# Kernel tuning notes

Hardware: AMD Instinct MI355X
Metric: run time of the kernel (lower is better)

The kernel has to match this reference:

```python
import jax, jax.numpy as jnp
import numpy as np

N_EX, N_KC, D, HID, NHEADS = 10000, 500, 128, 128, 2
B, S = 256, 500
ALPHA = 0.2
NEG = -9e15


def setup_inputs() -> dict:
    key = jax.random.key(0)
    ks = jax.random.split(key, 24)
    sc = 0.1
    inp = {
        "adj_exercise_kc": jax.random.randint(ks[0], (N_EX, N_KC), 0, 2, dtype=jnp.int32),
        "kc_data": jax.random.randint(ks[1], (B, S), 0, N_KC).astype(jnp.int64),
        "exercise_data": jax.random.randint(ks[2], (B, S), 0, N_EX + 1).astype(jnp.int64),
        "exercise_respond_data": jax.random.randint(ks[3], (B, S), 0, 2 * N_EX + 1).astype(jnp.int64),
        "target": jax.random.randint(ks[4], (B * (S - 1), 1), 0, 2).astype(jnp.float32),
        # learned parameters
        "ex_embed": jax.random.normal(ks[5], (N_EX, D)) * sc,
        "kc_embed": jax.random.normal(ks[6], (N_KC, D)) * sc,
        "W1": jax.random.normal(ks[7], (NHEADS, D, D)) * sc,        # per-head shared proj
        "a_att": jax.random.normal(ks[8], (NHEADS, 2 * D, 1)) * sc,  # attention vector
        "E": jax.random.normal(ks[9], (NHEADS, D, D)) * sc,
        "rd_w": jax.random.normal(ks[10], (NHEADS, D, 2 * D)) * sc,  # reduceDim (mode 3)
        "rd_b": jnp.zeros((NHEADS, D)),
        "w_ih": jax.random.normal(ks[11], (4 * HID, 2 * D)) * sc,
        "w_hh": jax.random.normal(ks[12], (4 * HID, HID)) * sc,
        "b_ih": jnp.zeros((4 * HID,)),
        "b_hh": jnp.zeros((4 * HID,)),
        "fc1_w": jax.random.normal(ks[13], (HID, D + HID)) * sc,
        "fc1_b": jnp.zeros((HID,)),
        "fc2_w": jax.random.normal(ks[14], (1, HID)) * sc,
        "fc2_b": jnp.zeros((1,)),
    }
    return inp


def _gat_head(ex_h, kc_h, adj, W1h, ah, Eh, rdw, rdb):
    # mode == 3 GAT head. a_input @ a decomposes: e[i,j] = LReLU(exWh[i].a1 + kcWh[j].a2)
    kc_Wh = kc_h @ W1h                                   # [Nkc, D]
    ex_Wh = ex_h @ W1h                                   # [Nex, D]
    e = jax.nn.leaky_relu(ex_Wh @ ah[:D] + (kc_Wh @ ah[D:]).T, ALPHA)  # [Nex, Nkc]
    att = jax.nn.softmax(jnp.where(adj > 0, e, NEG), axis=1)
    new_kc = att @ kc_Wh                                 # [Nex, D]
    ex_Eh = ex_h @ Eh
    emb = jnp.concatenate([new_kc, new_kc * ex_Eh], axis=1) @ rdw.T + rdb
    return jax.nn.elu(emb)                               # [Nex, D]


def _lstm(x, w_ih, w_hh, b_ih, b_hh):
    # single-layer torch LSTM, gate order i,f,g,o
    b = x.shape[0]
    xg = jnp.einsum('bsi,gi->sbg', x, w_ih) + b_ih + b_hh  # [S,B,4H]

    def step(carry, xt):
        h, c = carry
        g = xt + h @ w_hh.T
        i, f, gg, o = jnp.split(g, 4, axis=-1)
        c = jax.nn.sigmoid(f) * c + jax.nn.sigmoid(i) * jnp.tanh(gg)
        h = jax.nn.sigmoid(o) * jnp.tanh(c)
        return (h, c), h

    init = (jnp.zeros((b, HID), x.dtype), jnp.zeros((b, HID), x.dtype))
    _, hs = jax.lax.scan(step, init, xg)
    return jnp.swapaxes(hs, 0, 1)                        # [B,S,H]


def _forward(adj, exercise_data, respond_data, target,
             ex_embed, kc_embed, W1, a_att, E, rd_w, rd_b,
             w_ih, w_hh, b_ih, b_hh, fc1_w, fc1_b, fc2_w, fc2_b):
    heads = jax.vmap(_gat_head, in_axes=(None, None, None, 0, 0, 0, 0, 0))(
        ex_embed, kc_embed, adj, W1, a_att, E, rd_w, rd_b)   # [NH, Nex, D]
    # torch: cat(dim=1).view(Nex, D, NH).mean(2) -> interleaved reshape of the concat
    cat = jnp.swapaxes(heads, 0, 1).reshape(N_EX, NHEADS * D)
    exercise_embedding = cat.reshape(N_EX, D, NHEADS).mean(-1)  # [Nex, D]

    emb0 = jnp.concatenate([jnp.zeros((1, D), exercise_embedding.dtype), exercise_embedding], 0)
    assess = emb0[exercise_data]                          # [B,S,D]

    zeros = jnp.zeros_like(exercise_embedding)
    resp_emb = jnp.concatenate([
        jnp.concatenate([zeros, exercise_embedding], -1),
        jnp.concatenate([exercise_embedding, zeros], -1)], 0)  # [2Nex, 2D]
    resp0 = jnp.concatenate([jnp.zeros((1, 2 * D), resp_emb.dtype), resp_emb], 0)
    lstm_input = resp0[respond_data]                      # [B,S,2D]

    learn = _lstm(lstm_input, w_ih, w_hh, b_ih, b_hh)[:, :S - 1, :]  # [B,S-1,H]
    assess = assess[:, 1:, :]                             # [B,S-1,D]

    y = jax.nn.relu(jnp.concatenate([learn, assess], -1) @ fc1_w.T + fc1_b)
    pred = (y @ fc2_w.T + fc2_b).reshape(-1)              # [B*(S-1)]
    t = target.reshape(-1)                                # all targets >= 0 => mask all-true
    # BCE with logits, mean reduction
    loss = jnp.mean(jnp.maximum(pred, 0) - pred * t + jnp.log1p(jnp.exp(-jnp.abs(pred))))
    return loss, jax.nn.sigmoid(pred), t


def reference(adj_exercise_kc, kc_data, exercise_data, exercise_respond_data, target,
              ex_embed, kc_embed, W1, a_att, E, rd_w, rd_b,
              w_ih, w_hh, b_ih, b_hh, fc1_w, fc1_b, fc2_w, fc2_b):
    del kc_data  # unused by the original forward body
    return _forward(adj_exercise_kc, exercise_data, exercise_respond_data, target,
                    ex_embed, kc_embed, W1, a_att, E, rd_w, rd_b,
                    w_ih, w_hh, b_ih, b_hh, fc1_w, fc1_b, fc2_w, fc2_b)
```

## Files before the change

kernel.cpp:

```cpp
#include <hip/hip_runtime.h>
#include <math.h>

#define N_EX 10000
#define N_KC 500
#define D 128
#define HID 128
#define BB 256
#define SS 500
#define NROWS 127744

typedef float vf4 __attribute__((ext_vector_type(4)));
typedef _Float16 hf2 __attribute__((ext_vector_type(2)));

__device__ __forceinline__ float sigm(float x) { return 1.f / (1.f + __expf(-x)); }
__device__ __forceinline__ float tanh_fast(float x) { return 1.f - 2.f / (1.f + __expf(2.f * x)); }

__device__ __forceinline__ hf2 u2h(unsigned v) { union { unsigned u; hf2 h; } x; x.u = v; return x.h; }

__device__ __forceinline__ float quad_sum(float x) {
    int a = __builtin_amdgcn_update_dpp(0, __float_as_int(x), 0xB1, 0xF, 0xF, true);
    x += __int_as_float(a);
    int b = __builtin_amdgcn_update_dpp(0, __float_as_int(x), 0x4E, 0xF, 0xF, true);
    x += __int_as_float(b);
    return x;
}

__global__ void k_precomp(const float* rd_w, const float* w_ih, const float* fc1_w,
                          const float* b_ih, const float* b_hh, const float* W1, const float* a_att,
                          const float* w_hh,
                          float* rd_wT, float* w_ihT0, float* w_ihT1,
                          float* fc1_AT, float* fc1_BT, float* v1,
                          unsigned short* wlstm16, float* projC) {
    int idx = blockIdx.x * blockDim.x + threadIdx.x;
    int stride = gridDim.x * blockDim.x;
    const int N1 = 2 * 256 * 128;
    const int N2 = 128 * 512;
    const int N3 = 128 * 512;
    const int N4 = 128 * 128;
    const int N5 = 128 * 128;
    const int N6 = 512;
    const int N7 = 256;
    const int N8 = 65536;
    int total = N1 + N2 + N3 + N4 + N5 + N6 + N7 + N8;
    for (int tt = idx; tt < total; tt += stride) {
        int u = tt;
        if (u < N1) {
            int h = u / (256 * 128); int rem = u % (256 * 128); int c = rem / 128; int dd = rem % 128;
            rd_wT[u] = rd_w[h * 128 * 256 + dd * 256 + c];
        } else if ((u -= N1) < N2) {
            int k = u / 512, g = u % 512; w_ihT0[u] = w_ih[g * 256 + k];
        } else if ((u -= N2) < N3) {
            int k = u / 512, g = u % 512; w_ihT1[u] = w_ih[g * 256 + 128 + k];
        } else if ((u -= N3) < N4) {
            int k = u / 128, j = u % 128; fc1_AT[u] = fc1_w[j * 256 + k];
        } else if ((u -= N4) < N5) {
            int k = u / 128, j = u % 128; fc1_BT[u] = fc1_w[j * 256 + 128 + k];
        } else if ((u -= N5) < N6) {
            projC[u] = b_ih[u] + b_hh[u];
        } else if ((u -= N6) < N7) {
            int h = u / 128, k = u % 128;
            const float* wr = W1 + h * 16384 + k * 128;
            const float* av = a_att + h * 256;
            float acc = 0.f;
            for (int d = 0; d < 128; ++d) acc += wr[d] * av[d];
            v1[u] = acc;
        } else {
            u -= N7;
            int x = u & 7;
            int t = (u >> 3) & 511;
            int i = u >> 12;
            int g = i >> 2, j = i & 3;
            int uu = t >> 2, q = t & 3;
            float val = w_hh[(g * 128 + uu) * 128 + q * 32 + j * 8 + x];
            ((_Float16*)wlstm16)[u] = (_Float16)val;
        }
    }
}

__global__ void k_kc(const float* kc_embed, const float* W1, const float* a_att,
                     float* kcWhT, float* s_kc) {
    int j = blockIdx.x, h = blockIdx.y, d = threadIdx.x;
    __shared__ float row[128];
    __shared__ float red[128];
    row[d] = kc_embed[j * 128 + d];
    __syncthreads();
    const float* w = W1 + h * 16384;
    float acc = 0.f;
    for (int k = 0; k < 128; ++k) acc += row[k] * w[k * 128 + d];
    kcWhT[((size_t)(h * 128 + d)) * 500 + j] = acc;
    red[d] = acc * a_att[h * 256 + 128 + d];
    __syncthreads();
    for (int s = 64; s > 0; s >>= 1) { if (d < s) red[d] += red[d + s]; __syncthreads(); }
    if (d == 0) s_kc[h * 500 + j] = red[0];
}

__global__ void k_sex(const float* ex_embed, const float* v1, float* s_ex) {
    int t = blockIdx.x * blockDim.x + threadIdx.x;
    if (t >= 2 * N_EX) return;
    int h = t / N_EX, i = t % N_EX;
    const float4* e4 = (const float4*)(ex_embed + (size_t)i * 128);
    const float4* v4 = (const float4*)(v1 + h * 128);
    float acc = 0.f;
    for (int k = 0; k < 32; ++k) {
        float4 a = e4[k], b = v4[k];
        acc += a.x * b.x + a.y * b.y + a.z * b.z + a.w * b.w;
    }
    s_ex[h * N_EX + i] = acc;
}

__global__ __launch_bounds__(256) void k_attnk(const int* adj, const float* s_ex, const float* s_kc,
                                               const float* kcWhT, float* new_kc) {
    int i0 = blockIdx.x * 8, t = threadIdx.x;
    __shared__ vf4 at4[2][1500];
    __shared__ float skc_l[2][500];
    float* at0 = (float*)at4[0];
    float* at1 = (float*)at4[1];
    for (int j = t; j < 1000; j += 256) ((float*)skc_l)[j] = s_kc[j];
    __syncthreads();
    {
        int lg = t >> 5, lane = t & 31;
        int i = i0 + lg;
        float sex0 = s_ex[i];
        float sex1 = s_ex[N_EX + i];
        const int* arow = adj + (size_t)i * 500;
        float lmax0 = -INFINITY, lmax1 = -INFINITY;
        for (int j = lane; j < 500; j += 32) {
            bool m = arow[j] > 0;
            float e0 = sex0 + skc_l[0][j];
            e0 = (e0 >= 0.f) ? e0 : 0.2f * e0;
            e0 = m ? e0 : -INFINITY;
            float e1 = sex1 + skc_l[1][j];
            e1 = (e1 >= 0.f) ? e1 : 0.2f * e1;
            e1 = m ? e1 : -INFINITY;
            at0[j * 12 + lg] = e0;
            at1[j * 12 + lg] = e1;
            lmax0 = fmaxf(lmax0, e0);
            lmax1 = fmaxf(lmax1, e1);
        }
#pragma unroll
        for (int m = 16; m > 0; m >>= 1) {
            lmax0 = fmaxf(lmax0, __shfl_xor(lmax0, m));
            lmax1 = fmaxf(lmax1, __shfl_xor(lmax1, m));
        }
        float lsum0 = 0.f, lsum1 = 0.f;
        for (int j = lane; j < 500; j += 32) {
            float w0 = __expf(at0[j * 12 + lg] - lmax0);
            float w1 = __expf(at1[j * 12 + lg] - lmax1);
            at0[j * 12 + lg] = w0;
            at1[j * 12 + lg] = w1;
            lsum0 += w0; lsum1 += w1;
        }
#pragma unroll
        for (int m = 16; m > 0; m >>= 1) {
            lsum0 += __shfl_xor(lsum0, m);
            lsum1 += __shfl_xor(lsum1, m);
        }
        float inv0 = 1.f / lsum0, inv1 = 1.f / lsum1;
        for (int j = lane; j < 500; j += 32) {
            at0[j * 12 + lg] *= inv0;
            at1[j * 12 + lg] *= inv1;
        }
    }
    __syncthreads();
    int d = t & 127, half = t >> 7;
    for (int h = 0; h < 2; ++h) {
        const float* at = (h == 0) ? at0 : at1;
        const float* kcwd = kcWhT + ((size_t)(h * 128 + d)) * 500;
        vf4 acc = {0.f, 0.f, 0.f, 0.f};
        for (int j4 = 0; j4 < 125; ++j4) {
            vf4 w = *(const vf4*)(kcwd + j4 * 4);
            vf4 a0 = *(const vf4*)(at + (j4 * 4 + 0) * 12 + half * 4);
            vf4 a1 = *(const vf4*)(at + (j4 * 4 + 1) * 12 + half * 4);
            vf4 a2 = *(const vf4*)(at + (j4 * 4 + 2) * 12 + half * 4);
            vf4 a3 = *(const vf4*)(at + (j4 * 4 + 3) * 12 + half * 4);
            acc += a0 * w.x + a1 * w.y + a2 * w.z + a3 * w.w;
        }
        new_kc[((size_t)h * N_EX + i0 + half * 4 + 0) * 128 + d] = acc.x;
        new_kc[((size_t)h * N_EX + i0 + half * 4 + 1) * 128 + d] = acc.y;
        new_kc[((size_t)h * N_EX + i0 + half * 4 + 2) * 128 + d] = acc.z;
        new_kc[((size_t)h * N_EX + i0 + half * 4 + 3) * 128 + d] = acc.w;
    }
}

__global__ __launch_bounds__(256) void k_gat2m(const float* new_kc, const float* ex_embed,
                                               const float* E, const float* rd_wT,
                                               const float* rd_b, float* emb_e) {
    int i0 = blockIdx.x * 8, t = threadIdx.x;
    int d = t & 127, half = t >> 7;
    __shared__ float exrT[128 * 8];
    __shared__ float nkT[2][128 * 8];
    __shared__ float prT[128 * 8];
    __shared__ float Hl[2][8 * 128];
    for (int idx = t; idx < 8 * 128; idx += 256) {
        int r = idx >> 7, k = idx & 127;
        exrT[k * 8 + r]   = ex_embed[(size_t)i0 * 128 + idx];
        nkT[0][k * 8 + r] = new_kc[((size_t)i0) * 128 + idx];
        nkT[1][k * 8 + r] = new_kc[((size_t)N_EX + i0) * 128 + idx];
    }
    __syncthreads();
    for (int h = 0; h < 2; ++h) {
        const float* Eh = E + h * 16384;
        const float* rt = rd_wT + h * 256 * 128;
        float rb = rd_b[h * 128 + d];
        vf4 acc2 = {0.f, 0.f, 0.f, 0.f};
        for (int k = 0; k < 128; ++k) {
            float ev = Eh[k * 128 + d];
            vf4 ex4 = *(const vf4*)(exrT + k * 8 + half * 4);
            acc2 += ex4 * ev;
        }
        {
            vf4 nk4 = *(const vf4*)(nkT[h] + d * 8 + half * 4);
            *(vf4*)(prT + d * 8 + half * 4) = nk4 * acc2;
        }
        __syncthreads();
        vf4 acc3 = {0.f, 0.f, 0.f, 0.f};
        for (int c = 0; c < 128; ++c) {
            float w = rt[c * 128 + d];
            vf4 nk4 = *(const vf4*)(nkT[h] + c * 8 + half * 4);
            acc3 += nk4 * w;
        }
        for (int c = 0; c < 128; ++c) {
            float w = rt[(128 + c) * 128 + d];
            vf4 pr4 = *(const vf4*)(prT + c * 8 + half * 4);
            acc3 += pr4 * w;
        }
#pragma unroll
        for (int r = 0; r < 4; ++r) {
            float v = ((r == 0) ? acc3.x : (r == 1) ? acc3.y : (r == 2) ? acc3.z : acc3.w) + rb;
            v = (v > 0.f) ? v : expm1f(v);
            Hl[h][(half * 4 + r) * 128 + d] = v;
        }
        __syncthreads();
    }
    for (int idx = t; idx < 8 * 128; idx += 256) {
        int r = idx >> 7, dd = idx & 127;
        int hs = dd >> 6;
        int c0 = (2 * dd) & 127, c1 = (2 * dd + 1) & 127;
        emb_e[((size_t)i0 + r) * 128 + dd] = 0.5f * (Hl[hs][r * 128 + c0] + Hl[hs][r * 128 + c1]);
    }
}

__global__ __launch_bounds__(512) void k_proj(const float* emb_e, const float* w_ihT0,
                                              const float* w_ihT1, const float* fc1_BT,
                                              const float* b_ih, const float* b_hh,
                                              float* projC, float* assessP) {
    int i0 = blockIdx.x * 16, g = threadIdx.x;
    float gbl = b_ih[g] + b_hh[g];
    __shared__ float er[16 * 128];
    for (int idx = g; idx < 16 * 128; idx += 512) er[idx] = emb_e[(size_t)i0 * 128 + idx];
    __syncthreads();
    float a0[16], a1[16];
#pragma unroll
    for (int r = 0; r < 16; ++r) { a0[r] = 0.f; a1[r] = 0.f; }
    for (int k = 0; k < 128; ++k) {
        float w0 = w_ihT0[k * 512 + g], w1 = w_ihT1[k * 512 + g];
#pragma unroll
        for (int r = 0; r < 16; ++r) { float e = er[r * 128 + k]; a0[r] += e * w0; a1[r] += e * w1; }
    }
    for (int r = 0; r < 16; ++r) {
        projC[((size_t)(1 + i0 + r)) * 512 + g]        = a1[r] + gbl;
        projC[((size_t)(1 + N_EX + i0 + r)) * 512 + g] = a0[r] + gbl;
    }
    if (g < 128) {
        float b[16];
#pragma unroll
        for (int r = 0; r < 16; ++r) b[r] = 0.f;
        for (int k = 0; k < 128; ++k) {
            float w = fc1_BT[k * 128 + g];
#pragma unroll
            for (int r = 0; r < 16; ++r) b[r] += er[r * 128 + k] * w;
        }
        for (int r = 0; r < 16; ++r) assessP[((size_t)i0 + r) * 128 + g] = b[r];
    }
}

__global__ __launch_bounds__(512, 2) void k_lstm(const uint4* __restrict__ w16,
                                                 const float* __restrict__ projC,
                                                 const int* __restrict__ respond,
                                                 unsigned short* __restrict__ learn16) {
    int b = blockIdx.x, t = threadIdx.x;
    int u = t >> 2, q = t & 3;
    __shared__ uint4 hbuf4[2][18];
    __shared__ int rrow[500];
    uint4 w[16];
#pragma unroll
    for (int i = 0; i < 16; ++i) w[i] = w16[i * 512 + t];
    for (int s = t; s < 500; s += 512) rrow[s] = respond[b * 500 + s];
    if (t < 36) { uint4 z = {0u, 0u, 0u, 0u}; ((uint4*)hbuf4)[t] = z; }
    float c = 0.f;
    __syncthreads();
    const float* pc0 = projC + (size_t)rrow[0] * 512;
    float x0n = pc0[u], x1n = pc0[128 + u], x2n = pc0[256 + u], x3n = pc0[384 + u];
    for (int s = 0; s < 500; ++s) {
        int par = s & 1;
        float x0 = x0n, x1 = x1n, x2 = x2n, x3 = x3n;
        if (s < 499) {
            const float* pc = projC + (size_t)rrow[s + 1] * 512;
            x0n = pc[u]; x1n = pc[128 + u]; x2n = pc[256 + u]; x3n = pc[384 + u];
        }
        const uint4* hsegp = (const uint4*)((const unsigned short*)hbuf4[par] + q * 32);
        uint4 h4[4];
#pragma unroll
        for (int j = 0; j < 4; ++j) h4[j] = hsegp[j];
        float p0 = 0.f, p1 = 0.f, p2 = 0.f, p3 = 0.f;
#pragma unroll
        for (int j = 0; j < 4; ++j) {
            hf2 ha = u2h(h4[j].x), hb = u2h(h4[j].y), hc = u2h(h4[j].z), hd = u2h(h4[j].w);
            uint4 w0 = w[j], w1 = w[4 + j], w2 = w[8 + j], w3 = w[12 + j];
            p0 = __builtin_amdgcn_fdot2(u2h(w0.x), ha, p0, false);
            p0 = __builtin_amdgcn_fdot2(u2h(w0.y), hb, p0, false);
            p0 = __builtin_amdgcn_fdot2(u2h(w0.z), hc, p0, false);
            p0 = __builtin_amdgcn_fdot2(u2h(w0.w), hd, p0, false);
            p1 = __builtin_amdgcn_fdot2(u2h(w1.x), ha, p1, false);
            p1 = __builtin_amdgcn_fdot2(u2h(w1.y), hb, p1, false);
            p1 = __builtin_amdgcn_fdot2(u2h(w1.z), hc, p1, false);
            p1 = __builtin_amdgcn_fdot2(u2h(w1.w), hd, p1, false);
            p2 = __builtin_amdgcn_fdot2(u2h(w2.x), ha, p2, false);
            p2 = __builtin_amdgcn_fdot2(u2h(w2.y), hb, p2, false);
            p2 = __builtin_amdgcn_fdot2(u2h(w2.z), hc, p2, false);
            p2 = __builtin_amdgcn_fdot2(u2h(w2.w), hd, p2, false);
            p3 = __builtin_amdgcn_fdot2(u2h(w3.x), ha, p3, false);
            p3 = __builtin_amdgcn_fdot2(u2h(w3.y), hb, p3, false);
            p3 = __builtin_amdgcn_fdot2(u2h(w3.z), hc, p3, false);
            p3 = __builtin_amdgcn_fdot2(u2h(w3.w), hd, p3, false);
        }
        float gi = quad_sum(p0) + x0;
        float gf = quad_sum(p1) + x1;
        float gG = quad_sum(p2) + x2;
        float go = quad_sum(p3) + x3;
        float ii = sigm(gi), ff = sigm(gf), tg = tanh_fast(gG), oo = sigm(go);
        c = ff * c + ii * tg;
        float hh = oo * tanh_fast(c);
        if (q == 0) {
            union { unsigned short us; _Float16 hf; } cv; cv.hf = (_Float16)hh;
            ((unsigned short*)hbuf4[par ^ 1])[u] = cv.us;
            if (s < 499) learn16[((size_t)b * 499 + s) * 128 + u] = cv.us;
        }
        __syncthreads();
    }
}

__global__ __launch_bounds__(256) void k_mlp(const unsigned short* __restrict__ learn16,
                                             const float* __restrict__ assessP,
                                             const float* __restrict__ fc1_AT,
                                             const float* __restrict__ fc1_b,
                                             const float* __restrict__ fc2_w,
                                             const float* __restrict__ fc2_b,
                                             const int* __restrict__ exercise_data,
                                             const float* __restrict__ target,
                                             float* __restrict__ out,
                                             float* __restrict__ loss_accum) {
    int tile = blockIdx.x;
    int t = threadIdx.x;
    int jg = t & 31, rg = t >> 5;
    __shared__ float A_lds[64 * 128];
    __shared__ float x_lds[64 * 64];
    __shared__ float red[8];
    float4 acc[8];
#pragma unroll
    for (int r = 0; r < 8; ++r) acc[r] = make_float4(0.f, 0.f, 0.f, 0.f);
    int row0 = tile * 64;
    for (int kc = 0; kc < 2; ++kc) {
        for (int idx = t; idx < 64 * 128; idx += 256) A_lds[idx] = fc1_AT[kc * 64 * 128 + idx];
        for (int idx = t; idx < 64 * 32; idx += 256) {
            int r = idx >> 5, k2 = idx & 31;
            unsigned pv = *(const unsigned*)(learn16 + ((size_t)row0 + r) * 128 + kc * 64 + k2 * 2);
            hf2 hp = u2h(pv);
            x_lds[(r << 6) + k2 * 2]     = (float)hp.x;
            x_lds[(r << 6) + k2 * 2 + 1] = (float)hp.y;
        }
        __syncthreads();
        const float4* A4 = (const float4*)A_lds;
        const float4* x4 = (const float4*)x_lds;
#pragma unroll 4
        for (int k4 = 0; k4 < 16; ++k4) {
            float4 av[4];
#pragma unroll
            for (int kk = 0; kk < 4; ++kk) av[kk] = A4[(k4 * 4 + kk) * 32 + jg];
#pragma unroll
            for (int r = 0; r < 8; ++r) {
                float4 xv = x4[(rg * 8 + r) * 16 + k4];
                acc[r].x += xv.x * av[0].x + xv.y * av[1].x + xv.z * av[2].x + xv.w * av[3].x;
                acc[r].y += xv.x * av[0].y + xv.y * av[1].y + xv.z * av[2].y + xv.w * av[3].y;
                acc[r].z += xv.x * av[0].z + xv.y * av[1].z + xv.z * av[2].z + xv.w * av[3].z;
                acc[r].w += xv.x * av[0].w + xv.y * av[1].w + xv.z * av[2].w + xv.w * av[3].w;
            }
        }
        __syncthreads();
    }
    int j = jg * 4;
    float4 b1 = *(const float4*)(fc1_b + j);
    float4 f2 = *(const float4*)(fc2_w + j);
    float fb2 = fc2_b[0];
    float lloss = 0.f;
#pragma unroll
    for (int r = 0; r < 8; ++r) {
        int n = row0 + rg * 8 + r;
        int b = n / 499;
        int sidx = n - b * 499;
        int e = exercise_data[b * 500 + sidx + 1];
        float4 aP = make_float4(0.f, 0.f, 0.f, 0.f);
        if (e > 0) aP = *(const float4*)(assessP + (size_t)(e - 1) * 128 + j);
        float y0 = acc[r].x + aP.x + b1.x; y0 = y0 > 0.f ? y0 : 0.f;
        float y1 = acc[r].y + aP.y + b1.y; y1 = y1 > 0.f ? y1 : 0.f;
        float y2 = acc[r].z + aP.z + b1.z; y2 = y2 > 0.f ? y2 : 0.f;
        float y3 = acc[r].w + aP.w + b1.w; y3 = y3 > 0.f ? y3 : 0.f;
        float s = y0 * f2.x + y1 * f2.y + y2 * f2.z + y3 * f2.w;
#pragma unroll
        for (int m = 16; m > 0; m >>= 1) s += __shfl_xor(s, m, 32);
        if (jg == 0) {
            float p = s + fb2;
            float tg = target[n];
            out[1 + n] = 1.f / (1.f + expf(-p));
            float ab = fabsf(p);
            lloss += fmaxf(p, 0.f) - p * tg + log1pf(expf(-ab));
            out[1 + NROWS + n] = tg;
        }
    }
    if (jg == 0) red[rg] = lloss;
    __syncthreads();
    if (t == 0) {
        float sum = 0.f;
#pragma unroll
        for (int g = 0; g < 8; ++g) sum += red[g];
        atomicAdd(loss_accum, sum);
    }
}

__global__ void k_final(const float* loss_accum, float* out) {
    out[0] = loss_accum[0] * (1.f / (float)NROWS);
}

extern "C" void kernel_launch(void* const* d_in, const int* in_sizes, int n_in,
                              void* d_out, int out_size, void* d_ws, size_t ws_size,
                              hipStream_t stream) {
    const int* adj            = (const int*)d_in[0];
    const int* exercise_data  = (const int*)d_in[2];
    const int* respond        = (const int*)d_in[3];
    const float* target       = (const float*)d_in[4];
    const float* ex_embed     = (const float*)d_in[5];
    const float* kc_embed     = (const float*)d_in[6];
    const float* W1           = (const float*)d_in[7];
    const float* a_att        = (const float*)d_in[8];
    const float* E            = (const float*)d_in[9];
    const float* rd_w         = (const float*)d_in[10];
    const float* rd_b         = (const float*)d_in[11];
    const float* w_ih         = (const float*)d_in[12];
    const float* w_hh         = (const float*)d_in[13];
    const float* b_ih         = (const float*)d_in[14];
    const float* b_hh         = (const float*)d_in[15];
    const float* fc1_w        = (const float*)d_in[16];
    const float* fc1_b        = (const float*)d_in[17];
    const float* fc2_w        = (const float*)d_in[18];
    const float* fc2_b        = (const float*)d_in[19];
    float* out = (float*)d_out;

    float* ws = (float*)d_ws;
    size_t off = 0;
    auto alloc = [&](size_t n) { float* p = ws + off; off += (n + 3) & ~(size_t)3; return p; };
    float* kcWhT   = alloc(2 * 128 * 500);
    float* s_kc    = alloc(1000);
    float* v1      = alloc(256);
    float* s_ex    = alloc(2 * N_EX);
    float* emb_e   = alloc((size_t)N_EX * 128);
    float* rd_wT   = alloc(2 * 256 * 128);
    float* w_ihT0  = alloc(128 * 512);
    float* w_ihT1  = alloc(128 * 512);
    float* fc1_AT  = alloc(128 * 128);
    float* fc1_BT  = alloc(128 * 128);
    float* wlstm   = alloc(32768);
    float* new_kc  = alloc((size_t)2 * N_EX * 128);
    float* projC   = alloc((size_t)(2 * N_EX + 1) * 512);
    float* assessP = alloc((size_t)N_EX * 128);
    float* learn16 = alloc((size_t)BB * 499 * 64);
    float* loss_accum = alloc(4);

    k_precomp<<<256, 256, 0, stream>>>(rd_w, w_ih, fc1_w, b_ih, b_hh, W1, a_att, w_hh,
                                       rd_wT, w_ihT0, w_ihT1, fc1_AT, fc1_BT, v1,
                                       (unsigned short*)wlstm, projC);
    k_kc<<<dim3(500, 2), 128, 0, stream>>>(kc_embed, W1, a_att, kcWhT, s_kc);
    k_sex<<<79, 256, 0, stream>>>(ex_embed, v1, s_ex);
    k_attnk<<<N_EX / 8, 256, 0, stream>>>(adj, s_ex, s_kc, kcWhT, new_kc);
    k_gat2m<<<N_EX / 8, 256, 0, stream>>>(new_kc, ex_embed, E, rd_wT, rd_b, emb_e);
    k_proj<<<N_EX / 16, 512, 0, stream>>>(emb_e, w_ihT0, w_ihT1, fc1_BT, b_ih, b_hh,
                                          projC, assessP);
    hipMemsetAsync(loss_accum, 0, sizeof(float), stream);
    k_lstm<<<BB, 512, 0, stream>>>((const uint4*)wlstm, projC, respond,
                                   (unsigned short*)learn16);
    k_mlp<<<NROWS / 64, 256, 0, stream>>>((const unsigned short*)learn16, assessP, fc1_AT,
                                          fc1_b, fc2_w, fc2_b,
                                          exercise_data, target, out, loss_accum);
    k_final<<<1, 1, 0, stream>>>(loss_accum, out);
}
```

Measured before the change: 800.7 us.

## Use fp16 MFMA for input projection and MLP, interleave gate columns

The scalar fp32 input-projection kernel (k_proj) and the fc1 MLP kernel are replaced with tiled fp16 MFMA 16x16x32 kernels. Their weights are pre-converted to fp16 and emb_e is now written as fp16. The projected gate columns are interleaved per hidden unit, so the LSTM loads its four gate pre-activations with one float4 load instead of four scalar loads. This cuts FLOP-bound ALU time in the projection and MLP stages at the cost of fp16 rounding on the embeddings and weights.

```diff
diff --git a/kernel.cpp b/kernel.cpp
--- a/kernel.cpp
+++ b/kernel.cpp
@@ -11,6 +11,8 @@
 
 typedef float vf4 __attribute__((ext_vector_type(4)));
 typedef _Float16 hf2 __attribute__((ext_vector_type(2)));
+typedef _Float16 hf8 __attribute__((ext_vector_type(8)));
+typedef float f32x4 __attribute__((ext_vector_type(4)));
 
 __device__ __forceinline__ float sigm(float x) { return 1.f / (1.f + __expf(-x)); }
 __device__ __forceinline__ float tanh_fast(float x) { return 1.f - 2.f / (1.f + __expf(2.f * x)); }
@@ -28,36 +30,43 @@
 __global__ void k_precomp(const float* rd_w, const float* w_ih, const float* fc1_w,
                           const float* b_ih, const float* b_hh, const float* W1, const float* a_att,
                           const float* w_hh,
-                          float* rd_wT, float* w_ihT0, float* w_ihT1,
-                          float* fc1_AT, float* fc1_BT, float* v1,
+                          float* rd_wT, unsigned short* w_all16, unsigned short* fc1A16,
+                          float* gb512, float* v1,
                           unsigned short* wlstm16, float* projC) {
     int idx = blockIdx.x * blockDim.x + threadIdx.x;
     int stride = gridDim.x * blockDim.x;
     const int N1 = 2 * 256 * 128;
-    const int N2 = 128 * 512;
-    const int N3 = 128 * 512;
-    const int N4 = 128 * 128;
-    const int N5 = 128 * 128;
-    const int N6 = 512;
+    const int NW = 1152 * 128;
+    const int NF = 128 * 128;
+    const int NG = 512;
     const int N7 = 256;
     const int N8 = 65536;
-    int total = N1 + N2 + N3 + N4 + N5 + N6 + N7 + N8;
+    int total = N1 + NW + NF + NG + N7 + N8;
     for (int tt = idx; tt < total; tt += stride) {
         int u = tt;
         if (u < N1) {
             int h = u / (256 * 128); int rem = u % (256 * 128); int c = rem / 128; int dd = rem % 128;
             rd_wT[u] = rd_w[h * 128 * 256 + dd * 256 + c];
-        } else if ((u -= N1) < N2) {
-            int k = u / 512, g = u % 512; w_ihT0[u] = w_ih[g * 256 + k];
-        } else if ((u -= N2) < N3) {
-            int k = u / 512, g = u % 512; w_ihT1[u] = w_ih[g * 256 + 128 + k];
-        } else if ((u -= N3) < N4) {
-            int k = u / 128, j = u % 128; fc1_AT[u] = fc1_w[j * 256 + k];
-        } else if ((u -= N4) < N5) {
-            int k = u / 128, j = u % 128; fc1_BT[u] = fc1_w[j * 256 + 128 + k];
-        } else if ((u -= N5) < N6) {
-            projC[u] = b_ih[u] + b_hh[u];
-        } else if ((u -= N6) < N7) {
+        } else if ((u -= N1) < NW) {
+            int n = u >> 7, k = u & 127;
+            float val;
+            if (n < 512) {
+                int c = n; val = w_ih[((c & 3) * 128 + (c >> 2)) * 256 + 128 + k];
+            } else if (n < 1024) {
+                int c = n - 512; val = w_ih[((c & 3) * 128 + (c >> 2)) * 256 + k];
+            } else {
+                int j = n - 1024; val = fc1_w[j * 256 + 128 + k];
+            }
+            ((_Float16*)w_all16)[u] = (_Float16)val;
+        } else if ((u -= NW) < NF) {
+            int j = u >> 7, k = u & 127;
+            ((_Float16*)fc1A16)[u] = (_Float16)fc1_w[j * 256 + k];
+        } else if ((u -= NF) < NG) {
+            int c = u;
+            float v = b_ih[(c & 3) * 128 + (c >> 2)] + b_hh[(c & 3) * 128 + (c >> 2)];
+            gb512[c] = v;
+            projC[c] = v;
+        } else if ((u -= NG) < N7) {
             int h = u / 128, k = u % 128;
             const float* wr = W1 + h * 16384 + k * 128;
             const float* av = a_att + h * 256;
@@ -184,7 +193,7 @@
 
 __global__ __launch_bounds__(256) void k_gat2m(const float* new_kc, const float* ex_embed,
                                                const float* E, const float* rd_wT,
-                                               const float* rd_b, float* emb_e) {
+                                               const float* rd_b, _Float16* emb16) {
     int i0 = blockIdx.x * 8, t = threadIdx.x;
     int d = t & 127, half = t >> 7;
     __shared__ float exrT[128 * 8];
@@ -236,41 +245,73 @@
         int r = idx >> 7, dd = idx & 127;
         int hs = dd >> 6;
         int c0 = (2 * dd) & 127, c1 = (2 * dd + 1) & 127;
-        emb_e[((size_t)i0 + r) * 128 + dd] = 0.5f * (Hl[hs][r * 128 + c0] + Hl[hs][r * 128 + c1]);
-    }
-}
-
-__global__ __launch_bounds__(512) void k_proj(const float* emb_e, const float* w_ihT0,
-                                              const float* w_ihT1, const float* fc1_BT,
-                                              const float* b_ih, const float* b_hh,
-                                              float* projC, float* assessP) {
-    int i0 = blockIdx.x * 16, g = threadIdx.x;
-    float gbl = b_ih[g] + b_hh[g];
-    __shared__ float er[16 * 128];
-    for (int idx = g; idx < 16 * 128; idx += 512) er[idx] = emb_e[(size_t)i0 * 128 + idx];
-    __syncthreads();
-    float a0[16], a1[16];
-#pragma unroll
-    for (int r = 0; r < 16; ++r) { a0[r] = 0.f; a1[r] = 0.f; }
-    for (int k = 0; k < 128; ++k) {
-        float w0 = w_ihT0[k * 512 + g], w1 = w_ihT1[k * 512 + g];
-#pragma unroll
-        for (int r = 0; r < 16; ++r) { float e = er[r * 128 + k]; a0[r] += e * w0; a1[r] += e * w1; }
-    }
-    for (int r = 0; r < 16; ++r) {
-        projC[((size_t)(1 + i0 + r)) * 512 + g]        = a1[r] + gbl;
-        projC[((size_t)(1 + N_EX + i0 + r)) * 512 + g] = a0[r] + gbl;
-    }
-    if (g < 128) {
-        float b[16];
-#pragma unroll
-        for (int r = 0; r < 16; ++r) b[r] = 0.f;
-        for (int k = 0; k < 128; ++k) {
-            float w = fc1_BT[k * 128 + g];
-#pragma unroll
-            for (int r = 0; r < 16; ++r) b[r] += er[r * 128 + k] * w;
-        }
-        for (int r = 0; r < 16; ++r) assessP[((size_t)i0 + r) * 128 + g] = b[r];
+        emb16[((size_t)i0 + r) * 128 + dd] =
+            (_Float16)(0.5f * (Hl[hs][r * 128 + c0] + Hl[hs][r * 128 + c1]));
+    }
+}
+
+__global__ __launch_bounds__(256) void k_projM(const unsigned short* __restrict__ emb16,
+                                               const unsigned short* __restrict__ w_all16,
+                                               const float* __restrict__ gb512,
+                                               float* __restrict__ projC,
+                                               float* __restrict__ assessP) {
+    int mt = blockIdx.x, nt = blockIdx.y;
+    int i0 = mt * 64, n0 = nt * 64;
+    int t = threadIdx.x;
+    __shared__ _Float16 Al[64 * 136];
+    __shared__ _Float16 Bl[64 * 136];
+    for (int idx = t; idx < 512; idx += 256) {
+        int r = idx >> 3, sg = idx & 7;
+        int gi = i0 + r; if (gi >= N_EX) gi = N_EX - 1;
+        *(uint4*)(Al + r * 136 + sg * 8) = *(const uint4*)(emb16 + (size_t)gi * 128 + sg * 8);
+    }
+    for (int idx = t; idx < 512; idx += 256) {
+        int r = idx >> 3, sg = idx & 7;
+        *(uint4*)(Bl + r * 136 + sg * 8) = *(const uint4*)(w_all16 + (size_t)(n0 + r) * 128 + sg * 8);
+    }
+    __syncthreads();
+    int w = t >> 6, l = t & 63, quad = l >> 4, lx = l & 15;
+    const _Float16* ab = Al + ((w << 4) + lx) * 136 + (quad << 3);
+    hf8 a0 = *(const hf8*)(ab);
+    hf8 a1 = *(const hf8*)(ab + 32);
+    hf8 a2 = *(const hf8*)(ab + 64);
+    hf8 a3 = *(const hf8*)(ab + 96);
+    f32x4 acc[4];
+#pragma unroll
+    for (int ct = 0; ct < 4; ++ct) {
+        const _Float16* bb = Bl + ((ct << 4) + lx) * 136 + (quad << 3);
+        f32x4 c = {0.f, 0.f, 0.f, 0.f};
+        c = __builtin_amdgcn_mfma_f32_16x16x32_f16(a0, *(const hf8*)(bb),      c, 0, 0, 0);
+        c = __builtin_amdgcn_mfma_f32_16x16x32_f16(a1, *(const hf8*)(bb + 32), c, 0, 0, 0);
+        c = __builtin_amdgcn_mfma_f32_16x16x32_f16(a2, *(const hf8*)(bb + 64), c, 0, 0, 0);
+        c = __builtin_amdgcn_mfma_f32_16x16x32_f16(a3, *(const hf8*)(bb + 96), c, 0, 0, 0);
+        acc[ct] = c;
+    }
+    int rbase = i0 + (w << 4) + (quad << 2);
+    if (nt < 16) {
+        size_t rowbase = (nt < 8) ? 1 : (size_t)(1 + N_EX);
+        int cc = n0 & 511;
+#pragma unroll
+        for (int ct = 0; ct < 4; ++ct) {
+            int col = cc + (ct << 4) + lx;
+            float gb = gb512[col];
+#pragma unroll
+            for (int reg = 0; reg < 4; ++reg) {
+                int gi = rbase + reg;
+                if (gi < N_EX) projC[(rowbase + gi) * 512 + col] = acc[ct][reg] + gb;
+            }
+        }
+    } else {
+        int cc = n0 - 1024;
+#pragma unroll
+        for (int ct = 0; ct < 4; ++ct) {
+            int col = cc + (ct << 4) + lx;
+#pragma unroll
+            for (int reg = 0; reg < 4; ++reg) {
+                int gi = rbase + reg;
+                if (gi < N_EX) assessP[(size_t)gi * 128 + col] = acc[ct][reg];
+            }
+        }
     }
 }
 
@@ -289,15 +330,11 @@
     if (t < 36) { uint4 z = {0u, 0u, 0u, 0u}; ((uint4*)hbuf4)[t] = z; }
     float c = 0.f;
     __syncthreads();
-    const float* pc0 = projC + (size_t)rrow[0] * 512;
-    float x0n = pc0[u], x1n = pc0[128 + u], x2n = pc0[256 + u], x3n = pc0[384 + u];
+    vf4 xg_n = ((const vf4*)(projC + (size_t)rrow[0] * 512))[u];
     for (int s = 0; s < 500; ++s) {
         int par = s & 1;
-        float x0 = x0n, x1 = x1n, x2 = x2n, x3 = x3n;
-        if (s < 499) {
-            const float* pc = projC + (size_t)rrow[s + 1] * 512;
-            x0n = pc[u]; x1n = pc[128 + u]; x2n = pc[256 + u]; x3n = pc[384 + u];
-        }
+        vf4 xg = xg_n;
+        if (s < 499) xg_n = ((const vf4*)(projC + (size_t)rrow[s + 1] * 512))[u];
         const uint4* hsegp = (const uint4*)((const unsigned short*)hbuf4[par] + q * 32);
         uint4 h4[4];
 #pragma unroll
@@ -324,10 +361,10 @@
             p3 = __builtin_amdgcn_fdot2(u2h(w3.z), hc, p3, false);
             p3 = __builtin_amdgcn_fdot2(u2h(w3.w), hd, p3, false);
         }
-        float gi = quad_sum(p0) + x0;
-        float gf = quad_sum(p1) + x1;
-        float gG = quad_sum(p2) + x2;
-        float go = quad_sum(p3) + x3;
+        float gi = quad_sum(p0) + xg.x;
+        float gf = quad_sum(p1) + xg.y;
+        float gG = quad_sum(p2) + xg.z;
+        float go = quad_sum(p3) + xg.w;
         float ii = sigm(gi), ff = sigm(gf), tg = tanh_fast(gG), oo = sigm(go);
         c = ff * c + ii * tg;
         float hh = oo * tanh_fast(c);
@@ -340,91 +377,93 @@
     }
 }
 
-__global__ __launch_bounds__(256) void k_mlp(const unsigned short* __restrict__ learn16,
-                                             const float* __restrict__ assessP,
-                                             const float* __restrict__ fc1_AT,
-                                             const float* __restrict__ fc1_b,
-                                             const float* __restrict__ fc2_w,
-                                             const float* __restrict__ fc2_b,
-                                             const int* __restrict__ exercise_data,
-                                             const float* __restrict__ target,
-                                             float* __restrict__ out,
-                                             float* __restrict__ loss_accum) {
+__global__ __launch_bounds__(256) void k_mlpM(const unsigned short* __restrict__ learn16,
+                                              const unsigned short* __restrict__ fc1A16,
+                                              const float* __restrict__ assessP,
+                                              const float* __restrict__ fc1_b,
+                                              const float* __restrict__ fc2_w,
+                                              const float* __restrict__ fc2_b,
+                                              const int* __restrict__ exercise_data,
+                                              const float* __restrict__ target,
+                                              float* __restrict__ out,
+                                              float* __restrict__ loss_accum) {
     int tile = blockIdx.x;
+    int row0 = tile * 64;
     int t = threadIdx.x;
-    int jg = t & 31, rg = t >> 5;
-    __shared__ float A_lds[64 * 128];
-    __shared__ float x_lds[64 * 64];
-    __shared__ float red[8];
-    float4 acc[8];
-#pragma unroll
-    for (int r = 0; r < 8; ++r) acc[r] = make_float4(0.f, 0.f, 0.f, 0.f);
-    int row0 = tile * 64;
-    for (int kc = 0; kc < 2; ++kc) {
-        for (int idx = t; idx < 64 * 128; idx += 256) A_lds[idx] = fc1_AT[kc * 64 * 128 + idx];
-        for (int idx = t; idx < 64 * 32; idx += 256) {
-            int r = idx >> 5, k2 = idx & 31;
-            unsigned pv = *(const unsigned*)(learn16 + ((size_t)row0 + r) * 128 + kc * 64 + k2 * 2);
-            hf2 hp = u2h(pv);
-            x_lds[(r << 6) + k2 * 2]     = (float)hp.x;
-            x_lds[(r << 6) + k2 * 2 + 1] = (float)hp.y;
-        }
-        __syncthreads();
-        const float4* A4 = (const float4*)A_lds;
-        const float4* x4 = (const float4*)x_lds;
-#pragma unroll 4
-        for (int k4 = 0; k4 < 16; ++k4) {
-            float4 av[4];
-#pragma unroll
-            for (int kk = 0; kk < 4; ++kk) av[kk] = A4[(k4 * 4 + kk) * 32 + jg];
-#pragma unroll
-            for (int r = 0; r < 8; ++r) {
-                float4 xv = x4[(rg * 8 + r) * 16 + k4];
-                acc[r].x += xv.x * av[0].x + xv.y * av[1].x + xv.z * av[2].x + xv.w * av[3].x;
-                acc[r].y += xv.x * av[0].y + xv.y * av[1].y + xv.z * av[2].y + xv.w * av[3].y;
-                acc[r].z += xv.x * av[0].z + xv.y * av[1].z + xv.z * av[2].z + xv.w * av[3].z;
-                acc[r].w += xv.x * av[0].w + xv.y * av[1].w + xv.z * av[2].w + xv.w * av[3].w;
-            }
-        }
-        __syncthreads();
-    }
-    int j = jg * 4;
-    float4 b1 = *(const float4*)(fc1_b + j);
-    float4 f2 = *(const float4*)(fc2_w + j);
+    __shared__ _Float16 Al[64 * 136];
+    __shared__ _Float16 Bl[128 * 136];
+    __shared__ float red[4];
+    for (int idx = t; idx < 512; idx += 256) {
+        int r = idx >> 3, sg = idx & 7;
+        *(uint4*)(Al + r * 136 + sg * 8) = *(const uint4*)(learn16 + ((size_t)row0 + r) * 128 + sg * 8);
+    }
+    for (int idx = t; idx < 1024; idx += 256) {
+        int r = idx >> 3, sg = idx & 7;
+        *(uint4*)(Bl + r * 136 + sg * 8) = *(const uint4*)(fc1A16 + r * 128 + sg * 8);
+    }
+    __syncthreads();
+    int w = t >> 6, l = t & 63, quad = l >> 4, lx = l & 15;
+    const _Float16* ab = Al + ((w << 4) + lx) * 136 + (quad << 3);
+    hf8 a0 = *(const hf8*)(ab);
+    hf8 a1 = *(const hf8*)(ab + 32);
+    hf8 a2 = *(const hf8*)(ab + 64);
+    hf8 a3 = *(const hf8*)(ab + 96);
+    f32x4 acc[8];
+#pragma unroll
+    for (int ct = 0; ct < 8; ++ct) {
+        const _Float16* bb = Bl + ((ct << 4) + lx) * 136 + (quad << 3);
+        f32x4 c = {0.f, 0.f, 0.f, 0.f};
+        c = __builtin_amdgcn_mfma_f32_16x16x32_f16(a0, *(const hf8*)(bb),      c, 0, 0, 0);
+        c = __builtin_amdgcn_mfma_f32_16x16x32_f16(a1, *(const hf8*)(bb + 32), c, 0, 0, 0);
+        c = __builtin_amdgcn_mfma_f32_16x16x32_f16(a2, *(const hf8*)(bb + 64), c, 0, 0, 0);
+        c = __builtin_amdgcn_mfma_f32_16x16x32_f16(a3, *(const hf8*)(bb + 96), c, 0, 0, 0);
+        acc[ct] = c;
+    }
+    int eidx[4];
+#pragma unroll
+    for (int reg = 0; reg < 4; ++reg) {
+        int n = row0 + (w << 4) + (quad << 2) + reg;
+        int b = n / 499, sidx = n - b * 499;
+        eidx[reg] = exercise_data[b * 500 + sidx + 1];
+    }
+    float rs[4] = {0.f, 0.f, 0.f, 0.f};
+#pragma unroll
+    for (int ct = 0; ct < 8; ++ct) {
+        int col = (ct << 4) + lx;
+        float b1v = fc1_b[col], f2v = fc2_w[col];
+#pragma unroll
+        for (int reg = 0; reg < 4; ++reg) {
+            float aP = (eidx[reg] > 0) ? assessP[(size_t)(eidx[reg] - 1) * 128 + col] : 0.f;
+            float y = acc[ct][reg] + aP + b1v;
+            y = y > 0.f ? y : 0.f;
+            rs[reg] += y * f2v;
+        }
+    }
+#pragma unroll
+    for (int reg = 0; reg < 4; ++reg) {
+        float s = rs[reg];
+        s += __shfl_xor(s, 1); s += __shfl_xor(s, 2); s += __shfl_xor(s, 4); s += __shfl_xor(s, 8);
+        rs[reg] = s;
+    }
     float fb2 = fc2_b[0];
     float lloss = 0.f;
-#pragma unroll
-    for (int r = 0; r < 8; ++r) {
-        int n = row0 + rg * 8 + r;
-        int b = n / 499;
-        int sidx = n - b * 499;
-        int e = exercise_data[b * 500 + sidx + 1];
-        float4 aP = make_float4(0.f, 0.f, 0.f, 0.f);
-        if (e > 0) aP = *(const float4*)(assessP + (size_t)(e - 1) * 128 + j);
-        float y0 = acc[r].x + aP.x + b1.x; y0 = y0 > 0.f ? y0 : 0.f;
-        float y1 = acc[r].y + aP.y + b1.y; y1 = y1 > 0.f ? y1 : 0.f;
-        float y2 = acc[r].z + aP.z + b1.z; y2 = y2 > 0.f ? y2 : 0.f;
-        float y3 = acc[r].w + aP.w + b1.w; y3 = y3 > 0.f ? y3 : 0.f;
-        float s = y0 * f2.x + y1 * f2.y + y2 * f2.z + y3 * f2.w;
-#pragma unroll
-        for (int m = 16; m > 0; m >>= 1) s += __shfl_xor(s, m, 32);
-        if (jg == 0) {
-            float p = s + fb2;
+    if (lx == 0) {
+#pragma unroll
+        for (int reg = 0; reg < 4; ++reg) {
+            int n = row0 + (w << 4) + (quad << 2) + reg;
+            float p = rs[reg] + fb2;
             float tg = target[n];
             out[1 + n] = 1.f / (1.f + expf(-p));
-            float ab = fabsf(p);
-            lloss += fmaxf(p, 0.f) - p * tg + log1pf(expf(-ab));
+            float ab2 = fabsf(p);
+            lloss += fmaxf(p, 0.f) - p * tg + log1pf(expf(-ab2));
             out[1 + NROWS + n] = tg;
         }
     }
-    if (jg == 0) red[rg] = lloss;
-    __syncthreads();
-    if (t == 0) {
-        float sum = 0.f;
-#pragma unroll
-        for (int g = 0; g < 8; ++g) sum += red[g];
-        atomicAdd(loss_accum, sum);
-    }
+    lloss += __shfl_xor(lloss, 16);
+    lloss += __shfl_xor(lloss, 32);
+    if (l == 0) red[w] = lloss;
+    __syncthreads();
+    if (t == 0) atomicAdd(loss_accum, red[0] + red[1] + red[2] + red[3]);
 }
 
 __global__ void k_final(const float* loss_accum, float* out) {
@@ -462,13 +501,12 @@
     float* s_kc    = alloc(1000);
     float* v1      = alloc(256);
     float* s_ex    = alloc(2 * N_EX);
-    float* emb_e   = alloc((size_t)N_EX * 128);
     float* rd_wT   = alloc(2 * 256 * 128);
-    float* w_ihT0  = alloc(128 * 512);
-    float* w_ihT1  = alloc(128 * 512);
-    float* fc1_AT  = alloc(128 * 128);
-    float* fc1_BT  = alloc(128 * 128);
     float* wlstm   = alloc(32768);
+    float* w_all16 = alloc(1152 * 64);
+    float* fc1A16  = alloc(8192);
+    float* gb512   = alloc(512);
+    float* emb16   = alloc((size_t)N_EX * 64);
     float* new_kc  = alloc((size_t)2 * N_EX * 128);
     float* projC   = alloc((size_t)(2 * N_EX + 1) * 512);
     float* assessP = alloc((size_t)N_EX * 128);
@@ -476,19 +514,21 @@
     float* loss_accum = alloc(4);
 
     k_precomp<<<256, 256, 0, stream>>>(rd_w, w_ih, fc1_w, b_ih, b_hh, W1, a_att, w_hh,
-                                       rd_wT, w_ihT0, w_ihT1, fc1_AT, fc1_BT, v1,
-                                       (unsigned short*)wlstm, projC);
+                                       rd_wT, (unsigned short*)w_all16, (unsigned short*)fc1A16,
+                                       gb512, v1, (unsigned short*)wlstm, projC);
     k_kc<<<dim3(500, 2), 128, 0, stream>>>(kc_embed, W1, a_att, kcWhT, s_kc);
     k_sex<<<79, 256, 0, stream>>>(ex_embed, v1, s_ex);
     k_attnk<<<N_EX / 8, 256, 0, stream>>>(adj, s_ex, s_kc, kcWhT, new_kc);
-    k_gat2m<<<N_EX / 8, 256, 0, stream>>>(new_kc, ex_embed, E, rd_wT, rd_b, emb_e);
-    k_proj<<<N_EX / 16, 512, 0, stream>>>(emb_e, w_ihT0, w_ihT1, fc1_BT, b_ih, b_hh,
-                                          projC, assessP);
+    k_gat2m<<<N_EX / 8, 256, 0, stream>>>(new_kc, ex_embed, E, rd_wT, rd_b, (_Float16*)emb16);
+    k_projM<<<dim3(157, 18), 256, 0, stream>>>((const unsigned short*)emb16,
+                                               (const unsigned short*)w_all16, gb512,
+                                               projC, assessP);
     hipMemsetAsync(loss_accum, 0, sizeof(float), stream);
     k_lstm<<<BB, 512, 0, stream>>>((const uint4*)wlstm, projC, respond,
                                    (unsigned short*)learn16);
-    k_mlp<<<NROWS / 64, 256, 0, stream>>>((const unsigned short*)learn16, assessP, fc1_AT,
-                                          fc1_b, fc2_w, fc2_b,
-                                          exercise_data, target, out, loss_accum);
+    k_mlpM<<<NROWS / 64, 256, 0, stream>>>((const unsigned short*)learn16,
+                                           (const unsigned short*)fc1A16, assessP,
+                                           fc1_b, fc2_w, fc2_b,
+                                           exercise_data, target, out, loss_accum);
     k_final<<<1, 1, 0, stream>>>(loss_accum, out);
 }
```

New measurement: 697.2 us. -12.9%, faster.
